# Optimization experiments

Measured on AMD Instinct MI355X. Metric: run time of the kernel, lower is better.

The kernel has to match this reference:

```python
import jax, jax.numpy as jnp
import numpy as np
import math

MAX_T = 10000
LEARNING_RATE = 0.01
GAUSS_CUTOFF = 0.001


def setup_inputs() -> dict:
    key = jax.random.key(0)
    k1, k2 = jax.random.split(key)
    x = jax.random.uniform(k1, (32, 3, 16, 16), dtype=jnp.float32)
    units = jax.random.uniform(k2, (64, 64, 768), dtype=jnp.float32)
    return {"x": x, "units": units, "t": 100}


def reference(x, units, t):
    # units: [G, G, C]; x: [B, c, h, w] with c*h*w == C; t: python int (step)
    G, _, C = units.shape
    B = x.shape[0]

    # scalar schedule (matches torch calc_kernel_size / temperature)
    deno = 1.0 / (0.9 * MAX_T / math.log(G))
    ksize = G * math.exp(-t * deno)
    sigma = 0.3 * ((ksize - 1) * 0.5 - 1) + 0.8
    temperature = math.exp(-(t * 2) / MAX_T)

    xf = x.reshape(B, 1, 1, C)                      # [B,1,1,C]
    feat_diff = units[None] - xf                    # [B,G,G,C]
    feat_dist = jnp.sum(feat_diff * feat_diff, axis=3)  # [B,G,G]

    # best-matching unit (flattened argmin, row-major -> (y, x))
    bmu = jnp.argmin(feat_dist.reshape(B, -1), axis=1)   # [B]
    by = (bmu // G).astype(jnp.float32)
    bx = (bmu % G).astype(jnp.float32)

    grid = jnp.arange(G, dtype=jnp.float32)
    pos_dist = ((grid[None, :, None] - by[:, None, None]) ** 2
                + (grid[None, None, :] - bx[:, None, None]) ** 2)  # [B,G,G]

    gaussian = jnp.exp(-pos_dist / (2.0 * sigma * sigma))
    gaussian = jnp.where(gaussian < GAUSS_CUTOFF, 0.0, gaussian)

    delta = jnp.mean(temperature * gaussian[..., None] * feat_diff, axis=0)  # [G,G,C]
    return units - LEARNING_RATE * delta
```

## Files before the change

### kernel.cpp

```cpp
#include <hip/hip_runtime.h>
#include <math.h>

#define G 64
#define GG 4096
#define C 768
#define B 32
#define LR 0.01f
#define CUTOFF 0.001f

__global__ __launch_bounds__(64) void som_dist(const float* __restrict__ x,
                                               const float* __restrict__ units,
                                               float* __restrict__ dist) {
    const int u0 = blockIdx.x * 4;
    const int lane = threadIdx.x;

    float4 uv[4][3];
#pragma unroll
    for (int u = 0; u < 4; ++u)
#pragma unroll
        for (int k = 0; k < 3; ++k)
            uv[u][k] = *(const float4*)(units + (size_t)(u0 + u) * C + 4 * lane + 256 * k);

    for (int b = 0; b < B; ++b) {
        float4 xv[3];
#pragma unroll
        for (int k = 0; k < 3; ++k)
            xv[k] = *(const float4*)(x + (size_t)b * C + 4 * lane + 256 * k);

        float acc0 = 0.f, acc1 = 0.f, acc2 = 0.f, acc3 = 0.f;
#pragma unroll
        for (int k = 0; k < 3; ++k) {
            float d;
            d = uv[0][k].x - xv[k].x; acc0 += d * d;
            d = uv[0][k].y - xv[k].y; acc0 += d * d;
            d = uv[0][k].z - xv[k].z; acc0 += d * d;
            d = uv[0][k].w - xv[k].w; acc0 += d * d;
            d = uv[1][k].x - xv[k].x; acc1 += d * d;
            d = uv[1][k].y - xv[k].y; acc1 += d * d;
            d = uv[1][k].z - xv[k].z; acc1 += d * d;
            d = uv[1][k].w - xv[k].w; acc1 += d * d;
            d = uv[2][k].x - xv[k].x; acc2 += d * d;
            d = uv[2][k].y - xv[k].y; acc2 += d * d;
            d = uv[2][k].z - xv[k].z; acc2 += d * d;
            d = uv[2][k].w - xv[k].w; acc2 += d * d;
            d = uv[3][k].x - xv[k].x; acc3 += d * d;
            d = uv[3][k].y - xv[k].y; acc3 += d * d;
            d = uv[3][k].z - xv[k].z; acc3 += d * d;
            d = uv[3][k].w - xv[k].w; acc3 += d * d;
        }
#pragma unroll
        for (int off = 32; off; off >>= 1) {
            acc0 += __shfl_xor(acc0, off);
            acc1 += __shfl_xor(acc1, off);
            acc2 += __shfl_xor(acc2, off);
            acc3 += __shfl_xor(acc3, off);
        }
        if (lane == 0) {
            dist[(size_t)b * GG + u0 + 0] = acc0;
            dist[(size_t)b * GG + u0 + 1] = acc1;
            dist[(size_t)b * GG + u0 + 2] = acc2;
            dist[(size_t)b * GG + u0 + 3] = acc3;
        }
    }
}

__global__ __launch_bounds__(256) void som_argmin(const float* __restrict__ dist,
                                                  int* __restrict__ bmu) {
    const int b = blockIdx.x;
    const int t = threadIdx.x;

    unsigned long long best = ~0ull;
    for (int i = t; i < GG; i += 256) {
        unsigned int bits = __float_as_uint(dist[(size_t)b * GG + i]);
        unsigned long long key = ((unsigned long long)bits << 32) | (unsigned int)i;
        best = best < key ? best : key;
    }
#pragma unroll
    for (int off = 32; off; off >>= 1) {
        unsigned long long o = __shfl_xor(best, off);
        best = best < o ? best : o;
    }
    __shared__ unsigned long long s[4];
    if ((t & 63) == 0) s[t >> 6] = best;
    __syncthreads();
    if (t == 0) {
        unsigned long long m01 = s[0] < s[1] ? s[0] : s[1];
        unsigned long long m23 = s[2] < s[3] ? s[2] : s[3];
        unsigned long long m = m01 < m23 ? m01 : m23;
        bmu[b] = (int)(m & 0xffffffffu);
    }
}

__global__ __launch_bounds__(256) void som_update(const float* __restrict__ x,
                                                  const float* __restrict__ units,
                                                  const int* __restrict__ bmu,
                                                  const int* __restrict__ t_ptr,
                                                  float* __restrict__ out) {
    const int u0 = blockIdx.x * 4;
    const int tid = threadIdx.x;

    const float tt = (float)t_ptr[0];
    const float deno = logf(64.0f) / 9000.0f;
    const float ksize = 64.0f * expf(-tt * deno);
    const float sigma = 0.3f * ((ksize - 1.0f) * 0.5f - 1.0f) + 0.8f;
    const float inv2s2 = 1.0f / (2.0f * sigma * sigma);
    const float temp = expf(-(tt * 2.0f) / 10000.0f);
    const float s = LR * temp / (float)B;

    __shared__ float w[4][B];
    __shared__ float Sg[4];
    if (tid < 4 * B) {
        const int u = tid >> 5, b = tid & 31;
        const int gu = u0 + u;
        const float gy = (float)(gu >> 6), gx = (float)(gu & 63);
        const int bm = bmu[b];
        const float by = (float)(bm >> 6), bx = (float)(bm & 63);
        const float pd = (gy - by) * (gy - by) + (gx - bx) * (gx - bx);
        float g = expf(-pd * inv2s2);
        if (g < CUTOFF) g = 0.0f;
        w[u][b] = g;
    }
    __syncthreads();
    if (tid < 4) {
        float sg = 0.f;
#pragma unroll
        for (int b = 0; b < B; ++b) sg += w[tid][b];
        Sg[tid] = sg;
    }
    __syncthreads();

#pragma unroll
    for (int k = 0; k < 3; ++k) {
        const int c = tid + 256 * k;
        float xb[B];
#pragma unroll
        for (int b = 0; b < B; ++b) xb[b] = x[(size_t)b * C + c];
#pragma unroll
        for (int u = 0; u < 4; ++u) {
            float acc = 0.f;
#pragma unroll
            for (int b = 0; b < B; ++b) acc += w[u][b] * xb[b];
            const int gu = u0 + u;
            const float uval = units[(size_t)gu * C + c];
            out[(size_t)gu * C + c] = uval * (1.0f - s * Sg[u]) + s * acc;
        }
    }
}

extern "C" void kernel_launch(void* const* d_in, const int* in_sizes, int n_in,
                              void* d_out, int out_size, void* d_ws, size_t ws_size,
                              hipStream_t stream) {
    const float* x = (const float*)d_in[0];
    const float* units = (const float*)d_in[1];
    const int* t = (const int*)d_in[2];
    float* out = (float*)d_out;

    float* dist = (float*)d_ws;
    int* bmu = (int*)((char*)d_ws + (size_t)GG * B * sizeof(float));

    som_dist<<<GG / 4, 64, 0, stream>>>(x, units, dist);
    som_argmin<<<B, 256, 0, stream>>>(dist, bmu);
    som_update<<<GG / 4, 256, 0, stream>>>(x, units, bmu, t, out);
}
```

Before: 108.0 us.

## Fuse distance and argmin via 64-bit atomicMin keys, widen update tiles

Merges the distance kernel and the argmin kernel. Each block computes distances for 16 units against 16 batch rows and folds them into packed (distance, index) keys. It reduces these in-wave and in shared memory, then applies a global 64-bit atomicMin into padded per-batch slots. This removes the dist workspace round trip and one launch but adds a memset launch. The per-lane cross-reduction is also restructured so each lane ends up holding one unit's sum. The update kernel now handles 8 units per block with a shared BMU decode, halving the grid and reusing the x loads across more units.

```diff
diff --git a/kernel.cpp b/kernel.cpp
--- a/kernel.cpp
+++ b/kernel.cpp
@@ -8,95 +8,100 @@
 #define LR 0.01f
 #define CUTOFF 0.001f
 
-__global__ __launch_bounds__(64) void som_dist(const float* __restrict__ x,
-                                               const float* __restrict__ units,
-                                               float* __restrict__ dist) {
-    const int u0 = blockIdx.x * 4;
-    const int lane = threadIdx.x;
+#define KEY_STRIDE 16
+#define KEY_BYTES (B * KEY_STRIDE * 8)
+
+__device__ __forceinline__ float reduce4(float a0, float a1, float a2, float a3,
+                                         int lane) {
+    float r01 = ((lane & 1) ? a1 : a0) + __shfl_xor(((lane & 1) ? a0 : a1), 1);
+    float r23 = ((lane & 1) ? a3 : a2) + __shfl_xor(((lane & 1) ? a2 : a3), 1);
+    float r   = ((lane & 2) ? r23 : r01) + __shfl_xor(((lane & 2) ? r01 : r23), 2);
+    r += __shfl_xor(r, 4);
+    r += __shfl_xor(r, 8);
+    r += __shfl_xor(r, 16);
+    r += __shfl_xor(r, 32);
+    return r;
+}
+
+__global__ __launch_bounds__(256) void som_dist_argmin(const float* __restrict__ x,
+                                                       const float* __restrict__ units,
+                                                       unsigned long long* __restrict__ gkeys) {
+    const int ub = blockIdx.x >> 1;
+    const int bh = blockIdx.x & 1;
+    const int u0 = ub * 16;
+    const int b0 = bh * 16;
+    const int wv = threadIdx.x >> 6;
+    const int lane = threadIdx.x & 63;
+    const int uw = u0 + 4 * wv;
 
     float4 uv[4][3];
 #pragma unroll
     for (int u = 0; u < 4; ++u)
 #pragma unroll
         for (int k = 0; k < 3; ++k)
-            uv[u][k] = *(const float4*)(units + (size_t)(u0 + u) * C + 4 * lane + 256 * k);
+            uv[u][k] = *(const float4*)(units + (size_t)(uw + u) * C + 4 * lane + 256 * k);
 
-    for (int b = 0; b < B; ++b) {
+    __shared__ unsigned long long lkey[4][16];
+
+#pragma unroll 4
+    for (int bi = 0; bi < 16; ++bi) {
+        const int b = b0 + bi;
         float4 xv[3];
 #pragma unroll
         for (int k = 0; k < 3; ++k)
             xv[k] = *(const float4*)(x + (size_t)b * C + 4 * lane + 256 * k);
 
-        float acc0 = 0.f, acc1 = 0.f, acc2 = 0.f, acc3 = 0.f;
+        float a0 = 0.f, a1 = 0.f, a2 = 0.f, a3 = 0.f;
 #pragma unroll
         for (int k = 0; k < 3; ++k) {
             float d;
-            d = uv[0][k].x - xv[k].x; acc0 += d * d;
-            d = uv[0][k].y - xv[k].y; acc0 += d * d;
-            d = uv[0][k].z - xv[k].z; acc0 += d * d;
-            d = uv[0][k].w - xv[k].w; acc0 += d * d;
-            d = uv[1][k].x - xv[k].x; acc1 += d * d;
-            d = uv[1][k].y - xv[k].y; acc1 += d * d;
-            d = uv[1][k].z - xv[k].z; acc1 += d * d;
-            d = uv[1][k].w - xv[k].w; acc1 += d * d;
-            d = uv[2][k].x - xv[k].x; acc2 += d * d;
-            d = uv[2][k].y - xv[k].y; acc2 += d * d;
-            d = uv[2][k].z - xv[k].z; acc2 += d * d;
-            d = uv[2][k].w - xv[k].w; acc2 += d * d;
-            d = uv[3][k].x - xv[k].x; acc3 += d * d;
-            d = uv[3][k].y - xv[k].y; acc3 += d * d;
-            d = uv[3][k].z - xv[k].z; acc3 += d * d;
-            d = uv[3][k].w - xv[k].w; acc3 += d * d;
+            d = uv[0][k].x - xv[k].x; a0 += d * d;
+            d = uv[0][k].y - xv[k].y; a0 += d * d;
+            d = uv[0][k].z - xv[k].z; a0 += d * d;
+            d = uv[0][k].w - xv[k].w; a0 += d * d;
+            d = uv[1][k].x - xv[k].x; a1 += d * d;
+            d = uv[1][k].y - xv[k].y; a1 += d * d;
+            d = uv[1][k].z - xv[k].z; a1 += d * d;
+            d = uv[1][k].w - xv[k].w; a1 += d * d;
+            d = uv[2][k].x - xv[k].x; a2 += d * d;
+            d = uv[2][k].y - xv[k].y; a2 += d * d;
+            d = uv[2][k].z - xv[k].z; a2 += d * d;
+            d = uv[2][k].w - xv[k].w; a2 += d * d;
+            d = uv[3][k].x - xv[k].x; a3 += d * d;
+            d = uv[3][k].y - xv[k].y; a3 += d * d;
+            d = uv[3][k].z - xv[k].z; a3 += d * d;
+            d = uv[3][k].w - xv[k].w; a3 += d * d;
         }
-#pragma unroll
-        for (int off = 32; off; off >>= 1) {
-            acc0 += __shfl_xor(acc0, off);
-            acc1 += __shfl_xor(acc1, off);
-            acc2 += __shfl_xor(acc2, off);
-            acc3 += __shfl_xor(acc3, off);
-        }
-        if (lane == 0) {
-            dist[(size_t)b * GG + u0 + 0] = acc0;
-            dist[(size_t)b * GG + u0 + 1] = acc1;
-            dist[(size_t)b * GG + u0 + 2] = acc2;
-            dist[(size_t)b * GG + u0 + 3] = acc3;
-        }
+        const float s = reduce4(a0, a1, a2, a3, lane);
+
+        unsigned long long key =
+            ((unsigned long long)__float_as_uint(s) << 32) |
+            (unsigned int)(uw + (lane & 3));
+        unsigned long long o;
+        o = __shfl_xor(key, 1); key = key < o ? key : o;
+        o = __shfl_xor(key, 2); key = key < o ? key : o;
+        if (lane == 0) lkey[wv][bi] = key;
     }
-}
+    __syncthreads();
 
-__global__ __launch_bounds__(256) void som_argmin(const float* __restrict__ dist,
-                                                  int* __restrict__ bmu) {
-    const int b = blockIdx.x;
-    const int t = threadIdx.x;
-
-    unsigned long long best = ~0ull;
-    for (int i = t; i < GG; i += 256) {
-        unsigned int bits = __float_as_uint(dist[(size_t)b * GG + i]);
-        unsigned long long key = ((unsigned long long)bits << 32) | (unsigned int)i;
-        best = best < key ? best : key;
-    }
-#pragma unroll
-    for (int off = 32; off; off >>= 1) {
-        unsigned long long o = __shfl_xor(best, off);
-        best = best < o ? best : o;
-    }
-    __shared__ unsigned long long s[4];
-    if ((t & 63) == 0) s[t >> 6] = best;
-    __syncthreads();
-    if (t == 0) {
-        unsigned long long m01 = s[0] < s[1] ? s[0] : s[1];
-        unsigned long long m23 = s[2] < s[3] ? s[2] : s[3];
+    if (threadIdx.x < 16) {
+        unsigned long long k0 = lkey[0][threadIdx.x];
+        unsigned long long k1 = lkey[1][threadIdx.x];
+        unsigned long long k2 = lkey[2][threadIdx.x];
+        unsigned long long k3 = lkey[3][threadIdx.x];
+        unsigned long long m01 = k0 < k1 ? k0 : k1;
+        unsigned long long m23 = k2 < k3 ? k2 : k3;
         unsigned long long m = m01 < m23 ? m01 : m23;
-        bmu[b] = (int)(m & 0xffffffffu);
+        atomicMin(&gkeys[(size_t)(b0 + threadIdx.x) * KEY_STRIDE], m);
     }
 }
 
 __global__ __launch_bounds__(256) void som_update(const float* __restrict__ x,
                                                   const float* __restrict__ units,
-                                                  const int* __restrict__ bmu,
+                                                  const unsigned long long* __restrict__ gkeys,
                                                   const int* __restrict__ t_ptr,
                                                   float* __restrict__ out) {
-    const int u0 = blockIdx.x * 4;
+    const int u0 = blockIdx.x * 8;
     const int tid = threadIdx.x;
 
     const float tt = (float)t_ptr[0];
@@ -107,21 +112,28 @@
     const float temp = expf(-(tt * 2.0f) / 10000.0f);
     const float s = LR * temp / (float)B;
 
-    __shared__ float w[4][B];
-    __shared__ float Sg[4];
-    if (tid < 4 * B) {
+    __shared__ float by_s[B], bx_s[B];
+    __shared__ float w[8][B];
+    __shared__ float Sg[8];
+
+    if (tid < B) {
+        const int idx = (int)(gkeys[(size_t)tid * KEY_STRIDE] & 0xffffffffu);
+        by_s[tid] = (float)(idx >> 6);
+        bx_s[tid] = (float)(idx & 63);
+    }
+    __syncthreads();
+
+    {
         const int u = tid >> 5, b = tid & 31;
         const int gu = u0 + u;
         const float gy = (float)(gu >> 6), gx = (float)(gu & 63);
-        const int bm = bmu[b];
-        const float by = (float)(bm >> 6), bx = (float)(bm & 63);
-        const float pd = (gy - by) * (gy - by) + (gx - bx) * (gx - bx);
-        float g = expf(-pd * inv2s2);
+        const float dy = gy - by_s[b], dx = gx - bx_s[b];
+        float g = expf(-(dy * dy + dx * dx) * inv2s2);
         if (g < CUTOFF) g = 0.0f;
         w[u][b] = g;
     }
     __syncthreads();
-    if (tid < 4) {
+    if (tid < 8) {
         float sg = 0.f;
 #pragma unroll
         for (int b = 0; b < B; ++b) sg += w[tid][b];
@@ -136,7 +148,7 @@
 #pragma unroll
         for (int b = 0; b < B; ++b) xb[b] = x[(size_t)b * C + c];
 #pragma unroll
-        for (int u = 0; u < 4; ++u) {
+        for (int u = 0; u < 8; ++u) {
             float acc = 0.f;
 #pragma unroll
             for (int b = 0; b < B; ++b) acc += w[u][b] * xb[b];
@@ -155,10 +167,9 @@
     const int* t = (const int*)d_in[2];
     float* out = (float*)d_out;
 
-    float* dist = (float*)d_ws;
-    int* bmu = (int*)((char*)d_ws + (size_t)GG * B * sizeof(float));
+    unsigned long long* gkeys = (unsigned long long*)d_ws;
 
-    som_dist<<<GG / 4, 64, 0, stream>>>(x, units, dist);
-    som_argmin<<<B, 256, 0, stream>>>(dist, bmu);
-    som_update<<<GG / 4, 256, 0, stream>>>(x, units, bmu, t, out);
+    hipMemsetAsync(gkeys, 0xFF, KEY_BYTES, stream);
+    som_dist_argmin<<<512, 256, 0, stream>>>(x, units, gkeys);
+    som_update<<<512, 256, 0, stream>>>(x, units, gkeys, t, out);
 }
```

Measured after the change: 107.6 us. No clear change (-0.4%).
